# Kernel optimization log

Measured on AMD Instinct MI355X. Metric: run time of the kernel, lower is better.

## Reference

```python
import jax, jax.numpy as jnp
import numpy as np

B, H, W, C, HEADS, SR = 4, 64, 64, 256, 8, 2
D = C // HEADS            # head dim = 32
SCALE = D ** -0.5
EPS = 1e-6


def _conv(x, w, stride, pad, groups):
    return jax.lax.conv_general_dilated(
        x, w, (stride, stride), [(pad, pad), (pad, pad)],
        feature_group_count=groups,
        dimension_numbers=('NCHW', 'OIHW', 'NCHW'))


def setup_inputs() -> dict:
    key = jax.random.key(0)
    ks = jax.random.split(key, 9)
    s = lambda fan: 1.0 / np.sqrt(fan)
    return {
        'x': jax.random.normal(ks[0], (B, H * W, C), jnp.float32),
        'dw_w': jax.random.normal(ks[1], (C, 1, 3, 3), jnp.float32) * s(9),
        'dw_b': jnp.zeros((C,), jnp.float32),
        'pw_w': jax.random.normal(ks[2], (C, C, 1, 1), jnp.float32) * s(C),
        'pw_b': jnp.zeros((C,), jnp.float32),
        'sr_w': jax.random.normal(ks[3], (C, 1, 3, 3), jnp.float32) * s(9),
        'ln_g': jnp.ones((C,), jnp.float32),
        'ln_b': jnp.zeros((C,), jnp.float32),
        'kv_w': jax.random.normal(ks[4], (2 * C, C), jnp.float32) * s(C),
        'kv_b': jnp.zeros((2 * C,), jnp.float32),
        'proj_w': jax.random.normal(ks[5], (C, C), jnp.float32) * s(C),
        'proj_b': jnp.zeros((C,), jnp.float32),
    }


def reference(x, dw_w, dw_b, pw_w, pw_b, sr_w, ln_g, ln_b, kv_w, kv_b, proj_w, proj_b):
    Bx, N, Cx = x.shape
    # Q path: depthwise-separable conv on the spatial layout
    xq = x.reshape(Bx, H, W, Cx).transpose(0, 3, 1, 2)          # (B,C,H,W)
    q = _conv(xq, dw_w, 1, 1, Cx) + dw_b[None, :, None, None]    # depthwise 3x3
    q = _conv(q, pw_w, 1, 0, 1) + pw_b[None, :, None, None]      # pointwise 1x1
    # 'b (h d) l w -> b h (l w) d'
    q = q.reshape(Bx, HEADS, D, H * W).transpose(0, 1, 3, 2)     # (B,h,N,d)

    # SR path for K/V: strided depthwise conv + LayerNorm
    x_ = _conv(xq, sr_w, SR, SR // 2, Cx)                        # (B,C,H/SR,W/SR)
    x_ = x_.reshape(Bx, Cx, -1).transpose(0, 2, 1)               # (B,M,C)
    mu = jnp.mean(x_, axis=-1, keepdims=True)
    var = jnp.mean(jnp.square(x_ - mu), axis=-1, keepdims=True)
    x_ = (x_ - mu) * jax.lax.rsqrt(var + EPS) * ln_g + ln_b

    kv = x_ @ kv_w.T + kv_b                                      # (B,M,2C)
    M = kv.shape[1]
    kv = kv.reshape(Bx, M, 2, HEADS, D).transpose(2, 0, 3, 1, 4) # (2,B,h,M,d)
    k, v = kv[0], kv[1]

    attn = jnp.einsum('bhnd,bhmd->bhnm', q, k) * SCALE           # (B,h,N,M)
    attn = jax.nn.softmax(attn, axis=-1)
    out = jnp.einsum('bhnm,bhmd->bhnd', attn, v)                 # (B,h,N,d)
    out = out.transpose(0, 2, 1, 3).reshape(Bx, N, Cx)           # (B,N,C)
    return out @ proj_w.T + proj_b
```

## Files before the change

### kernel.cpp

```cpp
#include <hip/hip_runtime.h>
#include <math.h>

#define BB 4
#define HH 64
#define WW 64
#define CC 256
#define NN 4096
#define MM 1024
#define LN_EPS 1e-6f
#define SLF (0.17677669529663687f * 1.4426950408889634f)

typedef __attribute__((ext_vector_type(8)))  short short8;
typedef __attribute__((ext_vector_type(16))) float f32x16;

__device__ __forceinline__ ushort f2bf(float f) {
  unsigned u = __builtin_bit_cast(unsigned, f);
  u += 0x7fffu + ((u >> 16) & 1u);
  return (ushort)(u >> 16);
}
__device__ __forceinline__ float bf2f(ushort h) {
  unsigned u = ((unsigned)h) << 16;
  return __builtin_bit_cast(float, u);
}
#if __has_builtin(__builtin_amdgcn_exp2f)
#define EXP2F(x) __builtin_amdgcn_exp2f(x)
#else
#define EXP2F(x) exp2f(x)
#endif

__global__ __launch_bounds__(256) void pre_fused(
    const float* __restrict__ x, const float* __restrict__ dw_w,
    const float* __restrict__ dw_b, const float* __restrict__ sr_w,
    const float* __restrict__ ln_g, const float* __restrict__ ln_b,
    ushort* __restrict__ q1b, ushort* __restrict__ xsr) {
  int bid = blockIdx.x;
  int c = threadIdx.x;
  if (bid < 4096) {
    int b = bid >> 10, m = bid & 1023;
    int my = m >> 5, mx = m & 31;
    const float* xb = x + (size_t)b * NN * CC + c;
    float acc = 0.f;
#pragma unroll
    for (int dy = 0; dy < 3; ++dy) {
      int iy = 2 * my + dy - 1;
      if (iy < 0 || iy >= HH) continue;
#pragma unroll
      for (int dx = 0; dx < 3; ++dx) {
        int ix = 2 * mx + dx - 1;
        if (ix < 0 || ix >= WW) continue;
        acc += xb[(size_t)(iy * WW + ix) * CC] * sr_w[c * 9 + dy * 3 + dx];
      }
    }
    float v1 = acc, v2 = acc * acc;
#pragma unroll
    for (int s = 1; s < 64; s <<= 1) {
      v1 += __shfl_xor(v1, s);
      v2 += __shfl_xor(v2, s);
    }
    __shared__ float r1[4], r2[4];
    int lane = c & 63, wv = c >> 6;
    if (lane == 0) { r1[wv] = v1; r2[wv] = v2; }
    __syncthreads();
    float s1 = r1[0] + r1[1] + r1[2] + r1[3];
    float s2 = r2[0] + r2[1] + r2[2] + r2[3];
    float mu = s1 * (1.f / 256.f);
    float var = s2 * (1.f / 256.f) - mu * mu;
    float yv = (acc - mu) * rsqrtf(var + LN_EPS) * ln_g[c] + ln_b[c];
    xsr[((size_t)b * MM + m) * CC + c] = f2bf(yv);
  } else {
    int id = bid - 4096;
    int b = id >> 7, yy = id & 127;
    int y = yy >> 1, hf = yy & 1;
    float wr[9];
#pragma unroll
    for (int i = 0; i < 9; ++i) wr[i] = dw_w[c * 9 + i];
    float bi = dw_b[c];
    const float* xb = x + (size_t)b * NN * CC + c;
    int x0 = hf * 32;
    bool okT = (y > 0), okB = (y < 63);
    float a0, a1, a2, b0, b1, b2;
    if (x0 == 0) {
      a0 = a1 = a2 = 0.f;
    } else {
      a0 = okT ? xb[(size_t)((y - 1) * 64 + x0 - 1) * CC] : 0.f;
      a1 = xb[(size_t)(y * 64 + x0 - 1) * CC];
      a2 = okB ? xb[(size_t)((y + 1) * 64 + x0 - 1) * CC] : 0.f;
    }
    b0 = okT ? xb[(size_t)((y - 1) * 64 + x0) * CC] : 0.f;
    b1 = xb[(size_t)(y * 64 + x0) * CC];
    b2 = okB ? xb[(size_t)((y + 1) * 64 + x0) * CC] : 0.f;
    ushort* ob = q1b + ((size_t)b * NN + y * 64) * CC + c;
#pragma unroll 8
    for (int xx = x0; xx < x0 + 32; ++xx) {
      float c0v, c1v, c2v;
      if (xx < 63) {
        c0v = okT ? xb[(size_t)((y - 1) * 64 + xx + 1) * CC] : 0.f;
        c1v = xb[(size_t)(y * 64 + xx + 1) * CC];
        c2v = okB ? xb[(size_t)((y + 1) * 64 + xx + 1) * CC] : 0.f;
      } else {
        c0v = c1v = c2v = 0.f;
      }
      float acc = bi;
      acc += a0 * wr[0] + b0 * wr[1] + c0v * wr[2];
      acc += a1 * wr[3] + b1 * wr[4] + c1v * wr[5];
      acc += a2 * wr[6] + b2 * wr[7] + c2v * wr[8];
      ob[(size_t)xx * CC] = f2bf(acc);
      a0 = b0; a1 = b1; a2 = b2;
      b0 = c0v; b1 = c1v; b2 = c2v;
    }
  }
}

__global__ __launch_bounds__(256) void gemm_qkv(
    const ushort* __restrict__ q1b, const ushort* __restrict__ xsr,
    const float* __restrict__ pw_w, const float* __restrict__ pw_b,
    const float* __restrict__ kv_w, const float* __restrict__ kv_b,
    ushort* __restrict__ qB, ushort* __restrict__ kB,
    ushort* __restrict__ vT) {
  __shared__ ushort smem[2][128 * 40];
  int bid = blockIdx.x;
  bool is0 = bid < 1024;
  const ushort* A;
  const float* W;
  const float* bias;
  int r0, c0;
  if (is0) {
    A = q1b; W = pw_w; bias = pw_b;
    r0 = (bid >> 2) * 64; c0 = (bid & 3) * 64;
  } else {
    int sid = bid - 1024;
    A = xsr; W = kv_w; bias = kv_b;
    r0 = (sid >> 3) * 64; c0 = (sid & 7) * 64;
  }
  const bool vmode = (!is0) && (c0 >= 256);

  int t = threadIdx.x;
  int lane = t & 63, w = t >> 6;
  int l31 = lane & 31, half = lane >> 5;
  int wr = w >> 1, wc = w & 1;
  int rowA = t >> 2, kq = (t & 3) * 8;

  f32x16 acc;
#pragma unroll
  for (int i = 0; i < 16; ++i) acc[i] = 0.f;

  short8 ra;
  float4 rw0, rw1;
  auto prefetch = [&](int kc) {
    ra = *(const short8*)&A[(size_t)(r0 + rowA) * 256 + kc + kq];
    const float* wp = &W[(size_t)(c0 + rowA) * 256 + kc + kq];
    rw0 = *(const float4*)wp;
    rw1 = *(const float4*)(wp + 4);
  };
  auto store = [&](ushort* buf) {
    *(short8*)&buf[rowA * 40 + kq] = ra;
    float vals[8] = {rw0.x, rw0.y, rw0.z, rw0.w, rw1.x, rw1.y, rw1.z, rw1.w};
    short8 hi;
#pragma unroll
    for (int j = 0; j < 8; ++j) hi[j] = (short)f2bf(vals[j]);
    *(short8*)&buf[64 * 40 + rowA * 40 + kq] = hi;
  };

  prefetch(0);
  store(smem[0]);
  __syncthreads();
  for (int i = 0; i < 8; ++i) {
    ushort* cur = smem[i & 1];
    ushort* nxt = smem[(i & 1) ^ 1];
    if (i < 7) prefetch((i + 1) * 32);
#pragma unroll
    for (int ks = 0; ks < 2; ++ks) {
      short8 af = *(const short8*)&cur[(wr * 32 + l31) * 40 + ks * 16 + half * 8];
      short8 wf = *(const short8*)&cur[64 * 40 + (wc * 32 + l31) * 40 + ks * 16 + half * 8];
      if (vmode)
        acc = __builtin_amdgcn_mfma_f32_32x32x16_bf16(wf, af, acc, 0, 0, 0);
      else
        acc = __builtin_amdgcn_mfma_f32_32x32x16_bf16(af, wf, acc, 0, 0, 0);
    }
    if (i < 7) store(nxt);
    __syncthreads();
  }

#pragma unroll
  for (int i = 0; i < 16; ++i) {
    int rl = (i & 3) + 8 * (i >> 2) + 4 * half;
    if (is0) {
      int r = r0 + wr * 32 + rl;
      int c = c0 + wc * 32 + l31;
      int b = r >> 12, n = r & 4095;
      int h = c >> 5, d = c & 31;
      qB[((size_t)(b * 8 + h) * NN + n) * 32 + d] =
          f2bf((acc[i] + bias[c]) * SLF);
    } else if (!vmode) {
      int r = r0 + wr * 32 + rl;
      int c = c0 + wc * 32 + l31;
      int b = r >> 10, m = r & 1023;
      int h = c >> 5, d = c & 31;
      kB[((size_t)(b * 8 + h) * MM + m) * 32 + d] = f2bf(acc[i] + bias[c]);
    } else {
      int c = c0 + wc * 32 + rl;
      int r = r0 + wr * 32 + l31;
      int b = r >> 10, m = r & 1023;
      int cv = c - 256;
      int h = cv >> 5, d = cv & 31;
      vT[((size_t)(b * 8 + h) * 32 + d) * MM + m] = f2bf(acc[i] + bias[c]);
    }
  }
}

__global__ __launch_bounds__(256, 4) void attn_mfma(
    const ushort* __restrict__ qB, const ushort* __restrict__ kB,
    const ushort* __restrict__ vT, ushort* __restrict__ aH,
    ushort* __restrict__ aL) {
  __shared__ ushort sKa[2][8][264];
  __shared__ ushort sVa[2][8][264];
  __shared__ ushort pB[4][4][512];
  int t = threadIdx.x;
  int lane = t & 63, w = t >> 6;
  int l31 = lane & 31, half = lane >> 5;
  int bh = blockIdx.x;
  int b = bh >> 3, h = bh & 7;
  int q0 = blockIdx.y * 128;

  const ushort* qrow = qB + ((size_t)bh * NN + q0 + w * 32 + l31) * 32;
  short8 bq0 = *(const short8*)(qrow + half * 8);
  short8 bq1 = *(const short8*)(qrow + 16 + half * 8);

  const ushort* kbase = kB + (size_t)bh * MM * 32;
  const ushort* vbase = vT + (size_t)bh * 32 * MM;
  int krow = t >> 2, kq = (t & 3) * 8;
  int vd = t >> 3, vmo = (t & 7) * 8;
  int kreg_idx = (krow >> 5) * 4 + (kq >> 4) * 2 + ((kq >> 3) & 1);
  int klane = (krow & 31) * 8;
  int vreg_idx = (vmo >> 4) * 2 + ((vmo >> 3) & 1);
  int vlane = vd * 8;

  short8 ones;
#pragma unroll
  for (int j = 0; j < 8; ++j) ones[j] = (short)0x3F80;

  short8 kreg = *(const short8*)&kbase[(size_t)krow * 32 + kq];
  short8 vreg = *(const short8*)&vbase[(size_t)vd * MM + vmo];
  *(short8*)&sKa[0][kreg_idx][klane] = kreg;
  *(short8*)&sVa[0][vreg_idx][vlane] = vreg;

  f32x16 o, lacc;
#pragma unroll
  for (int i = 0; i < 16; ++i) { o[i] = 0.f; lacc[i] = 0.f; }
  __syncthreads();

  for (int mc = 0; mc < 16; ++mc) {
    int cur = mc & 1, nxt = cur ^ 1;
    if (mc < 15) {
      int m0n = (mc + 1) * 64;
      kreg = *(const short8*)&kbase[(size_t)(m0n + krow) * 32 + kq];
      vreg = *(const short8*)&vbase[(size_t)vd * MM + m0n + vmo];
    }
    f32x16 st[2];
#pragma unroll
    for (int tt = 0; tt < 2; ++tt) {
      short8 a0 = *(const short8*)&sKa[cur][tt * 4 + 0 + half][l31 * 8];
      short8 a1 = *(const short8*)&sKa[cur][tt * 4 + 2 + half][l31 * 8];
      f32x16 z;
#pragma unroll
      for (int i = 0; i < 16; ++i) z[i] = 0.f;
      z = __builtin_amdgcn_mfma_f32_32x32x16_bf16(a0, bq0, z, 0, 0, 0);
      z = __builtin_amdgcn_mfma_f32_32x32x16_bf16(a1, bq1, z, 0, 0, 0);
      st[tt] = z;
    }

#pragma unroll
    for (int tt = 0; tt < 2; ++tt) {
#pragma unroll
      for (int rg = 0; rg < 4; ++rg) {
        float p0 = EXP2F(st[tt][rg * 4 + 0]);
        float p1 = EXP2F(st[tt][rg * 4 + 1]);
        float p2 = EXP2F(st[tt][rg * 4 + 2]);
        float p3 = EXP2F(st[tt][rg * 4 + 3]);
        uint2 pk;
        pk.x = __builtin_amdgcn_perm(__builtin_bit_cast(unsigned, p1),
                                     __builtin_bit_cast(unsigned, p0), 0x07060302);
        pk.y = __builtin_amdgcn_perm(__builtin_bit_cast(unsigned, p3),
                                     __builtin_bit_cast(unsigned, p2), 0x07060302);
        *(uint2*)&pB[w][2 * tt + (rg >> 1)][((rg & 1) * 32 + l31) * 8 + 4 * half] = pk;
      }
    }

#pragma unroll
    for (int kb = 0; kb < 4; ++kb) {
      short8 av = *(const short8*)&sVa[cur][kb * 2 + half][l31 * 8];
      short8 bp = *(const short8*)&pB[w][kb][lane * 8];
      o = __builtin_amdgcn_mfma_f32_32x32x16_bf16(av, bp, o, 0, 0, 0);
      lacc = __builtin_amdgcn_mfma_f32_32x32x16_bf16(ones, bp, lacc, 0, 0, 0);
    }

    if (mc < 15) {
      *(short8*)&sKa[nxt][kreg_idx][klane] = kreg;
      *(short8*)&sVa[nxt][vreg_idx][vlane] = vreg;
    }
    __syncthreads();
  }

  float inv = 1.f / lacc[0];
  size_t rbase = ((size_t)b * NN + q0 + w * 32 + l31) * 256 + h * 32;
#pragma unroll
  for (int rg = 0; rg < 4; ++rg) {
#pragma unroll
    for (int j = 0; j < 4; ++j) {
      float v = o[rg * 4 + j] * inv;
      ushort hi = f2bf(v);
      ushort lo = f2bf(v - bf2f(hi));
      int d = rg * 8 + half * 4 + j;
      aH[rbase + d] = hi;
      aL[rbase + d] = lo;
    }
  }
}

__global__ __launch_bounds__(256) void gemm_proj(
    const ushort* __restrict__ A, const ushort* __restrict__ A2,
    const float* __restrict__ W, const float* __restrict__ bias,
    float* __restrict__ out) {
  __shared__ ushort smem[4 * 64 * 40];
  constexpr int OA = 0, OA2 = 64 * 40, OW = 2 * 64 * 40, OW2 = 3 * 64 * 40;
  int bid = blockIdx.x;
  int r0 = (bid >> 2) * 64, c0 = (bid & 3) * 64;

  int t = threadIdx.x;
  int lane = t & 63, w = t >> 6;
  int l31 = lane & 31, half = lane >> 5;
  int wr = w >> 1, wc = w & 1;
  int rowA = t >> 2, kq = (t & 3) * 8;

  f32x16 acc;
#pragma unroll
  for (int i = 0; i < 16; ++i) acc[i] = 0.f;

  short8 ra, ra2;
  float4 rw0, rw1;
  auto prefetch = [&](int kc) {
    ra = *(const short8*)&A[(size_t)(r0 + rowA) * 256 + kc + kq];
    ra2 = *(const short8*)&A2[(size_t)(r0 + rowA) * 256 + kc + kq];
    const float* wp = &W[(size_t)(c0 + rowA) * 256 + kc + kq];
    rw0 = *(const float4*)wp;
    rw1 = *(const float4*)(wp + 4);
  };
  auto store = [&]() {
    *(short8*)&smem[OA + rowA * 40 + kq] = ra;
    *(short8*)&smem[OA2 + rowA * 40 + kq] = ra2;
    float vals[8] = {rw0.x, rw0.y, rw0.z, rw0.w, rw1.x, rw1.y, rw1.z, rw1.w};
    short8 hi, lo;
#pragma unroll
    for (int j = 0; j < 8; ++j) {
      hi[j] = (short)f2bf(vals[j]);
      lo[j] = (short)f2bf(vals[j] - bf2f((ushort)hi[j]));
    }
    *(short8*)&smem[OW + rowA * 40 + kq] = hi;
    *(short8*)&smem[OW2 + rowA * 40 + kq] = lo;
  };

  prefetch(0);
  store();
  __syncthreads();
  for (int i = 0; i < 8; ++i) {
    if (i < 7) prefetch((i + 1) * 32);
#pragma unroll
    for (int ks = 0; ks < 2; ++ks) {
      int ro = (wr * 32 + l31) * 40 + ks * 16 + half * 8;
      int co = (wc * 32 + l31) * 40 + ks * 16 + half * 8;
      short8 af = *(const short8*)&smem[OA + ro];
      short8 af2 = *(const short8*)&smem[OA2 + ro];
      short8 wf = *(const short8*)&smem[OW + co];
      short8 wf2 = *(const short8*)&smem[OW2 + co];
      acc = __builtin_amdgcn_mfma_f32_32x32x16_bf16(af, wf, acc, 0, 0, 0);
      acc = __builtin_amdgcn_mfma_f32_32x32x16_bf16(af2, wf, acc, 0, 0, 0);
      acc = __builtin_amdgcn_mfma_f32_32x32x16_bf16(af, wf2, acc, 0, 0, 0);
    }
    __syncthreads();
    if (i < 7) {
      store();
      __syncthreads();
    }
  }

#pragma unroll
  for (int i = 0; i < 16; ++i) {
    int rl = (i & 3) + 8 * (i >> 2) + 4 * half;
    int r = r0 + wr * 32 + rl;
    int c = c0 + wc * 32 + l31;
    out[(size_t)r * 256 + c] = acc[i] + bias[c];
  }
}

extern "C" void kernel_launch(void* const* d_in, const int* in_sizes, int n_in,
                              void* d_out, int out_size, void* d_ws, size_t ws_size,
                              hipStream_t stream) {
  const float* x      = (const float*)d_in[0];
  const float* dw_w   = (const float*)d_in[1];
  const float* dw_b   = (const float*)d_in[2];
  const float* pw_w   = (const float*)d_in[3];
  const float* pw_b   = (const float*)d_in[4];
  const float* sr_w   = (const float*)d_in[5];
  const float* ln_g   = (const float*)d_in[6];
  const float* ln_b   = (const float*)d_in[7];
  const float* kv_w   = (const float*)d_in[8];
  const float* kv_b   = (const float*)d_in[9];
  const float* proj_w = (const float*)d_in[10];
  const float* proj_b = (const float*)d_in[11];
  float* out = (float*)d_out;

  char* ws = (char*)d_ws;
  ushort* q1b = (ushort*)(ws);
  ushort* xsr = (ushort*)(ws + (8u << 20));
  ushort* qB  = (ushort*)(ws + (16u << 20));
  ushort* kBp = (ushort*)(ws + (24u << 20));
  ushort* vTp = (ushort*)(ws + (26u << 20));
  ushort* aH  = (ushort*)(ws + (28u << 20));
  ushort* aL  = (ushort*)(ws + (36u << 20));

  pre_fused<<<dim3(4608), 256, 0, stream>>>(x, dw_w, dw_b, sr_w, ln_g, ln_b,
                                            q1b, xsr);
  gemm_qkv<<<dim3(1536), 256, 0, stream>>>(q1b, xsr, pw_w, pw_b, kv_w, kv_b,
                                           qB, kBp, vTp);
  attn_mfma<<<dim3(32, 32), 256, 0, stream>>>(qB, kBp, vTp, aH, aL);
  gemm_proj<<<dim3(1024), 256, 0, stream>>>(aH, aL, proj_w, proj_b, out);
}
```

Before: 171.0 us.

## Load K/V MFMA fragments directly from global memory, dropping LDS staging and barriers

The attention kernel now has each wave load its own K and V MFMA operand fragments straight from global memory into registers, prefetching the next chunk after use. This removes the shared-memory double buffer for K/V and the per-iteration __syncthreads. Each of the four waves in a block now loads the same K/V data separately, so global/L2 traffic rises roughly fourfold and register use grows. The min-blocks-per-SM launch bound is also dropped, which may lower occupancy.

```diff
diff --git a/kernel.cpp b/kernel.cpp
--- a/kernel.cpp
+++ b/kernel.cpp
@@ -208,12 +208,10 @@
   }
 }
 
-__global__ __launch_bounds__(256, 4) void attn_mfma(
+__global__ __launch_bounds__(256) void attn_mfma(
     const ushort* __restrict__ qB, const ushort* __restrict__ kB,
     const ushort* __restrict__ vT, ushort* __restrict__ aH,
     ushort* __restrict__ aL) {
-  __shared__ ushort sKa[2][8][264];
-  __shared__ ushort sVa[2][8][264];
   __shared__ ushort pB[4][4][512];
   int t = threadIdx.x;
   int lane = t & 63, w = t >> 6;
@@ -226,47 +224,46 @@
   short8 bq0 = *(const short8*)(qrow + half * 8);
   short8 bq1 = *(const short8*)(qrow + 16 + half * 8);
 
-  const ushort* kbase = kB + (size_t)bh * MM * 32;
-  const ushort* vbase = vT + (size_t)bh * 32 * MM;
-  int krow = t >> 2, kq = (t & 3) * 8;
-  int vd = t >> 3, vmo = (t & 7) * 8;
-  int kreg_idx = (krow >> 5) * 4 + (kq >> 4) * 2 + ((kq >> 3) & 1);
-  int klane = (krow & 31) * 8;
-  int vreg_idx = (vmo >> 4) * 2 + ((vmo >> 3) & 1);
-  int vlane = vd * 8;
+  const ushort* kfrag = kB + (size_t)bh * MM * 32 + l31 * 32 + half * 8;
+  const ushort* vfrag = vT + (size_t)bh * 32 * MM + (size_t)l31 * MM + half * 8;
 
   short8 ones;
 #pragma unroll
   for (int j = 0; j < 8; ++j) ones[j] = (short)0x3F80;
 
-  short8 kreg = *(const short8*)&kbase[(size_t)krow * 32 + kq];
-  short8 vreg = *(const short8*)&vbase[(size_t)vd * MM + vmo];
-  *(short8*)&sKa[0][kreg_idx][klane] = kreg;
-  *(short8*)&sVa[0][vreg_idx][vlane] = vreg;
+  short8 ka[4], va[4];
+#pragma unroll
+  for (int tt = 0; tt < 2; ++tt)
+#pragma unroll
+    for (int ks = 0; ks < 2; ++ks)
+      ka[tt * 2 + ks] = *(const short8*)(kfrag + (size_t)tt * 32 * 32 + ks * 16);
+#pragma unroll
+  for (int kb = 0; kb < 4; ++kb)
+    va[kb] = *(const short8*)(vfrag + kb * 16);
 
   f32x16 o, lacc;
 #pragma unroll
   for (int i = 0; i < 16; ++i) { o[i] = 0.f; lacc[i] = 0.f; }
-  __syncthreads();
 
   for (int mc = 0; mc < 16; ++mc) {
-    int cur = mc & 1, nxt = cur ^ 1;
+    int m0n = (mc + 1) * 64;
+    f32x16 st[2];
+#pragma unroll
+    for (int tt = 0; tt < 2; ++tt) {
+      f32x16 z;
+#pragma unroll
+      for (int i = 0; i < 16; ++i) z[i] = 0.f;
+      z = __builtin_amdgcn_mfma_f32_32x32x16_bf16(ka[tt * 2 + 0], bq0, z, 0, 0, 0);
+      z = __builtin_amdgcn_mfma_f32_32x32x16_bf16(ka[tt * 2 + 1], bq1, z, 0, 0, 0);
+      st[tt] = z;
+    }
     if (mc < 15) {
-      int m0n = (mc + 1) * 64;
-      kreg = *(const short8*)&kbase[(size_t)(m0n + krow) * 32 + kq];
-      vreg = *(const short8*)&vbase[(size_t)vd * MM + m0n + vmo];
-    }
-    f32x16 st[2];
-#pragma unroll
-    for (int tt = 0; tt < 2; ++tt) {
-      short8 a0 = *(const short8*)&sKa[cur][tt * 4 + 0 + half][l31 * 8];
-      short8 a1 = *(const short8*)&sKa[cur][tt * 4 + 2 + half][l31 * 8];
-      f32x16 z;
-#pragma unroll
-      for (int i = 0; i < 16; ++i) z[i] = 0.f;
-      z = __builtin_amdgcn_mfma_f32_32x32x16_bf16(a0, bq0, z, 0, 0, 0);
-      z = __builtin_amdgcn_mfma_f32_32x32x16_bf16(a1, bq1, z, 0, 0, 0);
-      st[tt] = z;
+#pragma unroll
+      for (int tt = 0; tt < 2; ++tt)
+#pragma unroll
+        for (int ks = 0; ks < 2; ++ks)
+          ka[tt * 2 + ks] = *(const short8*)(kfrag + (size_t)m0n * 32 +
+                                             (size_t)tt * 32 * 32 + ks * 16);
     }
 
 #pragma unroll
@@ -288,17 +285,15 @@
 
 #pragma unroll
     for (int kb = 0; kb < 4; ++kb) {
-      short8 av = *(const short8*)&sVa[cur][kb * 2 + half][l31 * 8];
       short8 bp = *(const short8*)&pB[w][kb][lane * 8];
-      o = __builtin_amdgcn_mfma_f32_32x32x16_bf16(av, bp, o, 0, 0, 0);
+      o = __builtin_amdgcn_mfma_f32_32x32x16_bf16(va[kb], bp, o, 0, 0, 0);
       lacc = __builtin_amdgcn_mfma_f32_32x32x16_bf16(ones, bp, lacc, 0, 0, 0);
     }
-
     if (mc < 15) {
-      *(short8*)&sKa[nxt][kreg_idx][klane] = kreg;
-      *(short8*)&sVa[nxt][vreg_idx][vlane] = vreg;
-    }
-    __syncthreads();
+#pragma unroll
+      for (int kb = 0; kb < 4; ++kb)
+        va[kb] = *(const short8*)(vfrag + m0n + kb * 16);
+    }
   }
 
   float inv = 1.f / lacc[0];
```

Result: slower. 186.8 us (+9.3%).
